# Kernel tuning notes

Hardware: AMD Instinct MI355X
Metric: run time of the kernel (lower is better)

The kernel has to match this reference:

```python
import jax, jax.numpy as jnp
import numpy as np

B, S, H, F, E, N, K = 2, 4096, 1024, 3584, 8, 2, 2


def setup_inputs() -> dict:
    key = jax.random.key(0)
    ks = jax.random.split(key, 6)
    scale_h = 1.0 / np.sqrt(H)
    scale_f = 1.0 / np.sqrt(F)
    return {
        "hidden_states": jax.random.normal(ks[0], (B, S, H), dtype=jnp.float32),
        "gate_w": jax.random.normal(ks[1], (E, H), dtype=jnp.float32) * scale_h,
        "gate2_w": jax.random.normal(ks[2], (N, H), dtype=jnp.float32) * scale_h,
        "w1": jax.random.normal(ks[3], (E, F, H), dtype=jnp.float32) * scale_h,
        "w2": jax.random.normal(ks[4], (E, H, F), dtype=jnp.float32) * scale_f,
        "w3": jax.random.normal(ks[5], (E, F, H), dtype=jnp.float32) * scale_h,
    }


def reference(hidden_states, gate_w, gate2_w, w1, w2, w3):
    b, s, h = hidden_states.shape
    x = hidden_states.reshape(-1, h)  # [T, H]

    # Router: real gate + null-expert gate, concatenated
    router_logits = jnp.concatenate([x @ gate_w.T, x @ gate2_w.T], axis=1)  # [T, E+N]
    rw = jax.nn.softmax(router_logits.astype(jnp.float32), axis=1)
    top_w, sel = jax.lax.top_k(rw, K)  # [T, K]

    # Null experts (idx >= E) get their raw weight; real experts are renormalized
    mask = sel < E
    sw = top_w * mask
    denom = sw.sum(axis=-1, keepdims=True)
    denom = jnp.where(denom == 0, 1.0, denom)
    weights = (sw / denom + top_w * (~mask)).astype(x.dtype)  # [T, K]

    # Per-(token, real-expert) combine weight; null experts drop out (one_hot -> 0)
    combine = jnp.einsum("tke,tk->et", jax.nn.one_hot(sel, E, dtype=x.dtype), weights)  # [E, T]

    def body(acc, p):
        w1e, w2e, w3e, cw = p
        hgate = jax.nn.silu(x @ w1e.T) * (x @ w3e.T)  # [T, F]
        return acc + cw[:, None] * (hgate @ w2e.T), None

    out, _ = jax.lax.scan(body, jnp.zeros_like(x), (w1, w2, w3, combine))
    return out.reshape(b, s, h), router_logits
```

## Files before the change

kernel.cpp:

```cpp
#include <hip/hip_runtime.h>
#include <hip/hip_bf16.h>

namespace {

constexpr int T_TOK = 8192;
constexpr int HDIM  = 1024;
constexpr int FDIM  = 3584;
constexpr int CAP_ROWS = 17408;
constexpr int MAXMT = CAP_ROWS / 128;

typedef __bf16 bf16x8 __attribute__((ext_vector_type(8)));
typedef float  f32x4  __attribute__((ext_vector_type(4)));
typedef float  f32x16 __attribute__((ext_vector_type(16)));

#define CFENCE() asm volatile("" ::: "memory")

__device__ inline unsigned short f2bf(float f) {
  union { float f; unsigned u; } a; a.f = f;
  unsigned r = a.u + 0x7fffu + ((a.u >> 16) & 1u);
  return (unsigned short)(r >> 16);
}

typedef const __attribute__((address_space(1))) void* gptr_t;
typedef __attribute__((address_space(3))) void* lptr_t;
__device__ inline void gload_lds16(const void* g, void* l) {
  __builtin_amdgcn_global_load_lds((gptr_t)g, (lptr_t)l, 16, 0, 0);
}

#define MFMA32(a, b, c) __builtin_amdgcn_mfma_f32_32x32x16_bf16(a, b, c, 0, 0, 0)

__global__ __launch_bounds__(256) void k_router(
    const float* __restrict__ x, const float* __restrict__ gw,
    const float* __restrict__ gw2, float* __restrict__ logits_out,
    int* __restrict__ sel, float* __restrict__ wts)
{
  int t = blockIdx.x * 4 + (threadIdx.x >> 6);
  int lane = threadIdx.x & 63;
  if (t >= T_TOK) return;
  const float* xr = x + (size_t)t * HDIM;
  float acc[10];
#pragma unroll
  for (int e = 0; e < 10; ++e) acc[e] = 0.f;
#pragma unroll
  for (int it = 0; it < 4; ++it) {
    int base = it * 256 + lane * 4;
    float4 xv = *reinterpret_cast<const float4*>(xr + base);
#pragma unroll
    for (int e = 0; e < 8; ++e) {
      float4 g = *reinterpret_cast<const float4*>(gw + e * HDIM + base);
      acc[e] += xv.x * g.x + xv.y * g.y + xv.z * g.z + xv.w * g.w;
    }
#pragma unroll
    for (int e = 0; e < 2; ++e) {
      float4 g = *reinterpret_cast<const float4*>(gw2 + e * HDIM + base);
      acc[8 + e] += xv.x * g.x + xv.y * g.y + xv.z * g.z + xv.w * g.w;
    }
  }
#pragma unroll
  for (int e = 0; e < 10; ++e) {
#pragma unroll
    for (int off = 32; off > 0; off >>= 1)
      acc[e] += __shfl_xor(acc[e], off, 64);
  }
  if (lane == 0) {
    float* lo = logits_out + (size_t)t * 10;
#pragma unroll
    for (int e = 0; e < 10; ++e) lo[e] = acc[e];
    float mx = acc[0];
#pragma unroll
    for (int e = 1; e < 10; ++e) mx = fmaxf(mx, acc[e]);
    float p[10], s = 0.f;
#pragma unroll
    for (int e = 0; e < 10; ++e) { p[e] = __expf(acc[e] - mx); s += p[e]; }
    float inv = 1.f / s;
#pragma unroll
    for (int e = 0; e < 10; ++e) p[e] *= inv;
    int i0 = 0;
    for (int e = 1; e < 10; ++e) if (p[e] > p[i0]) i0 = e;
    int i1 = (i0 == 0) ? 1 : 0;
    for (int e = 0; e < 10; ++e) if (e != i0 && p[e] > p[i1]) i1 = e;
    float w0 = p[i0], w1 = p[i1];
    bool r0 = i0 < 8, r1 = i1 < 8;
    float den = (r0 ? w0 : 0.f) + (r1 ? w1 : 0.f);
    if (den == 0.f) den = 1.f;
    sel[t * 2]     = i0; wts[t * 2]     = r0 ? w0 / den : 0.f;
    sel[t * 2 + 1] = i1; wts[t * 2 + 1] = r1 ? w1 / den : 0.f;
  }
}

__global__ __launch_bounds__(256) void k_histseg(
    const int* __restrict__ sel, int* __restrict__ meta)
{
  __shared__ int part[256][8];
  __shared__ int s_tile0[9];
  int tid = threadIdx.x;
  int c[8];
#pragma unroll
  for (int e = 0; e < 8; ++e) c[e] = 0;
  for (int i = 0; i < 64; ++i) {
    int v = sel[i * 256 + tid];
#pragma unroll
    for (int e = 0; e < 8; ++e) c[e] += (v == e);
  }
#pragma unroll
  for (int e = 0; e < 8; ++e) part[tid][e] = c[e];
  __syncthreads();
  for (int s = 128; s >= 1; s >>= 1) {
    if (tid < s) {
#pragma unroll
      for (int e = 0; e < 8; ++e) part[tid][e] += part[tid + s][e];
    }
    __syncthreads();
  }
  if (tid == 0) {
    int off = 0;
    for (int e = 0; e < 8; ++e) {
      int cnt = part[0][e];
      meta[e] = cnt;
      meta[8 + e] = 0;
      meta[16 + e] = off;
      s_tile0[e] = off >> 7;
      off += (cnt + 127) & ~127;
    }
    meta[24] = off;
    meta[25] = off >> 7;
    s_tile0[8] = off >> 7;
  }
  __syncthreads();
  int nt = s_tile0[8];
  if (tid < nt) {
    int e = 0;
    while (s_tile0[e + 1] <= tid) ++e;
    meta[32 + tid] = e;
  }
}

__global__ __launch_bounds__(256) void k_zeropad(
    const int* __restrict__ meta, unsigned short* __restrict__ xg)
{
  int e = blockIdx.x >> 7, r = blockIdx.x & 127;
  int c = meta[e];
  int pad = (c + 127) & ~127;
  if (c + r >= pad) return;
  size_t row = (size_t)meta[16 + e] + c + r;
  reinterpret_cast<ushort4*>(xg + row * HDIM)[threadIdx.x] = ushort4{0, 0, 0, 0};
}

__global__ __launch_bounds__(256) void k_scatter(
    const float* __restrict__ x, const int* __restrict__ sel,
    int* __restrict__ meta, int* __restrict__ pair_row,
    unsigned short* __restrict__ xg)
{
  __shared__ int s_cnt[8];
  __shared__ int s_base[8];
  __shared__ int s_row[256];
  int tid = threadIdx.x;
  int pair0 = blockIdx.x * 256;
  if (tid < 8) s_cnt[tid] = 0;
  __syncthreads();
  int e = sel[pair0 + tid];
  int rank = -1;
  if (e < 8) rank = atomicAdd(&s_cnt[e], 1);
  __syncthreads();
  if (tid < 8) {
    int c = s_cnt[tid];
    s_base[tid] = c > 0 ? atomicAdd(&meta[8 + tid], c) : 0;
  }
  __syncthreads();
  int row = (e < 8) ? meta[16 + e] + s_base[e] + rank : -1;
  pair_row[pair0 + tid] = row;
  s_row[tid] = row;
  __syncthreads();
  int wid = tid >> 6, lane = tid & 63;
  for (int i = wid; i < 256; i += 4) {
    int r = s_row[i];
    if (r < 0) continue;
    const float* xr = x + (size_t)((pair0 + i) >> 1) * HDIM;
    unsigned short* dst = xg + (size_t)r * HDIM;
#pragma unroll
    for (int it = 0; it < 4; ++it) {
      int base = it * 256 + lane * 4;
      float4 v = *reinterpret_cast<const float4*>(xr + base);
      ushort4 o{f2bf(v.x), f2bf(v.y), f2bf(v.z), f2bf(v.w)};
      *reinterpret_cast<ushort4*>(dst + base) = o;
    }
  }
}

__global__ __launch_bounds__(256) void k_conv3(
    const float* __restrict__ s1, const float* __restrict__ s3,
    const float* __restrict__ s2,
    unsigned short* __restrict__ d1, unsigned short* __restrict__ d3,
    unsigned short* __restrict__ d2,
    long long total, long long rl13, long long ss13,
    long long rl2, long long ss2)
{
  long long i = ((long long)blockIdx.x * 256 + threadIdx.x) * 8;
  if (i >= total) return;
  const float* src; unsigned short* dst; long long rowlen, sstride;
  if (blockIdx.y == 0)      { src = s1; dst = d1; rowlen = rl13; sstride = ss13; }
  else if (blockIdx.y == 1) { src = s3; dst = d3; rowlen = rl13; sstride = ss13; }
  else                      { src = s2; dst = d2; rowlen = rl2;  sstride = ss2;  }
  const float* sp;
  if (rowlen == sstride) {
    sp = src + i;
  } else {
    long long r = i / rowlen, c = i - r * rowlen;
    sp = src + r * sstride + c;
  }
  float4 a = reinterpret_cast<const float4*>(sp)[0];
  float4 b = reinterpret_cast<const float4*>(sp)[1];
  ushort4* d = reinterpret_cast<ushort4*>(dst + i);
  d[0] = ushort4{f2bf(a.x), f2bf(a.y), f2bf(a.z), f2bf(a.w)};
  d[1] = ushort4{f2bf(b.x), f2bf(b.y), f2bf(b.z), f2bf(b.w)};
}

__global__ __launch_bounds__(256) void k_gemm1(
    const unsigned short* __restrict__ xg,
    const unsigned short* __restrict__ wc1,
    const unsigned short* __restrict__ wc3,
    unsigned short* __restrict__ hg,
    const int* __restrict__ meta, int Fc)
{
  __shared__ unsigned short As[128 * 64];
  __shared__ unsigned short B1s[64 * 64];
  __shared__ unsigned short B3s[64 * 64];

  int mt = blockIdx.y;
  if (mt >= meta[25]) return;
  int e = meta[32 + mt];
  int mrow0 = mt * 128;
  int fl0 = blockIdx.x * 64;

  int tid = threadIdx.x, wid = tid >> 6, lane = tid & 63;
  int l31 = lane & 31, lh = lane >> 5;
  int wm = wid >> 1, wn = wid & 1;

  f32x16 acc1[2], acc3[2];
#pragma unroll
  for (int m = 0; m < 2; ++m)
#pragma unroll
    for (int j = 0; j < 16; ++j) { acc1[m][j] = 0.f; acc3[m][j] = 0.f; }

  const unsigned short* w1p = wc1 + ((size_t)e * Fc + fl0) * HDIM;
  const unsigned short* w3p = wc3 + ((size_t)e * Fc + fl0) * HDIM;

  int srow = tid >> 3;
  int sc8  = tid & 7;

  for (int k0 = 0; k0 < HDIM; k0 += 64) {
#pragma unroll
    for (int i = 0; i < 4; ++i) {
      int row = i * 32 + srow;
      int c8 = sc8 ^ (row & 7);
      gload_lds16(xg + (size_t)(mrow0 + row) * HDIM + k0 + c8 * 8,
                  (char*)As + i * 4096 + wid * 1024);
    }
#pragma unroll
    for (int i = 0; i < 2; ++i) {
      int row = i * 32 + srow;
      int c8 = sc8 ^ (row & 7);
      gload_lds16(w1p + (size_t)row * HDIM + k0 + c8 * 8,
                  (char*)B1s + i * 4096 + wid * 1024);
      gload_lds16(w3p + (size_t)row * HDIM + k0 + c8 * 8,
                  (char*)B3s + i * 4096 + wid * 1024);
    }
    __syncthreads();

#pragma unroll
    for (int ks = 0; ks < 4; ++ks) {
      int rb = wn * 32 + l31;
      int kb_b = (ks * 32 + lh * 16) ^ ((rb & 7) << 4);
      bf16x8 b1 = *reinterpret_cast<const bf16x8*>((const char*)B1s + rb * 128 + kb_b);
      bf16x8 b3 = *reinterpret_cast<const bf16x8*>((const char*)B3s + rb * 128 + kb_b);
#pragma unroll
      for (int m = 0; m < 2; ++m) {
        int ra = wm * 64 + m * 32 + l31;
        int kb_a = (ks * 32 + lh * 16) ^ ((ra & 7) << 4);
        bf16x8 a = *reinterpret_cast<const bf16x8*>((const char*)As + ra * 128 + kb_a);
        acc1[m] = MFMA32(a, b1, acc1[m]);
        acc3[m] = MFMA32(a, b3, acc3[m]);
      }
    }
    __syncthreads();
  }

#pragma unroll
  for (int m = 0; m < 2; ++m) {
    int gcol = fl0 + wn * 32 + l31;
#pragma unroll
    for (int r = 0; r < 16; ++r) {
      int grow = mrow0 + wm * 64 + m * 32 + (r & 3) + 8 * (r >> 2) + 4 * lh;
      float s1 = acc1[m][r];
      float s3 = acc3[m][r];
      float h = s1 / (1.f + __expf(-s1)) * s3;
      hg[(size_t)grow * Fc + gcol] = f2bf(h);
    }
  }
}

__global__ __launch_bounds__(256) void k_gemm2(
    const unsigned short* __restrict__ hg,
    const unsigned short* __restrict__ wc2,
    float* __restrict__ yrows, const int* __restrict__ meta,
    int Fc, int first)
{
  __shared__ __attribute__((aligned(128))) char lds[65536];

  int mt = blockIdx.y;
  if (mt >= meta[25]) return;
  int e = meta[32 + mt];
  int mrow0 = mt * 128;
  int hcol0 = blockIdx.x * 128;

  int tid = threadIdx.x, wid = tid >> 6, lane = tid & 63;
  int lr = lane & 15, lg = lane >> 4;
  int wm = wid >> 1, wn = wid & 1;

  f32x4 acc[4][4];
  const f32x4 zero = {0.f, 0.f, 0.f, 0.f};
#pragma unroll
  for (int m = 0; m < 4; ++m)
#pragma unroll
    for (int n = 0; n < 4; ++n) acc[m][n] = zero;

  const unsigned short* w2p = wc2 + ((size_t)e * HDIM + hcol0) * Fc;

  int srow = tid >> 3;
  int c8 = (tid & 7) ^ (srow & 7);

  const unsigned short* pa[4];
  const unsigned short* pb[4];
#pragma unroll
  for (int i = 0; i < 4; ++i) {
    pa[i] = hg + (size_t)(mrow0 + i * 32 + srow) * Fc + c8 * 8;
    pb[i] = w2p + (size_t)(i * 32 + srow) * Fc + c8 * 8;
  }

  auto STAGE = [&](int buf) {
    char* base = lds + buf * 32768;
#pragma unroll
    for (int i = 0; i < 4; ++i) {
      gload_lds16(pa[i], base + i * 4096 + wid * 1024);
      pa[i] += 64;
      gload_lds16(pb[i], base + 16384 + i * 4096 + wid * 1024);
      pb[i] += 64;
    }
  };

  auto COMPUTE = [&](int buf) {
    const char* base = lds + buf * 32768;
#pragma unroll
    for (int kk = 0; kk < 2; ++kk) {
      bf16x8 a[4], b[4];
#pragma unroll
      for (int m = 0; m < 4; ++m) {
        int r = wm * 64 + m * 16 + lr;
        int off = r * 128 + ((kk * 64 + lg * 16) ^ ((r & 7) << 4));
        a[m] = *reinterpret_cast<const bf16x8*>(base + off);
      }
#pragma unroll
      for (int n = 0; n < 4; ++n) {
        int r = wn * 64 + n * 16 + lr;
        int off = r * 128 + ((kk * 64 + lg * 16) ^ ((r & 7) << 4));
        b[n] = *reinterpret_cast<const bf16x8*>(base + 16384 + off);
      }
#pragma unroll
      for (int m = 0; m < 4; ++m)
#pragma unroll
        for (int n = 0; n < 4; ++n)
          acc[m][n] = __builtin_amdgcn_mfma_f32_16x16x32_bf16(a[m], b[n], acc[m][n], 0, 0, 0);
    }
  };

  int NT = Fc / 64;
  int cur = 0;
  STAGE(0);
#pragma unroll 1
  for (int t = 0; t < NT - 1; ++t) {
    STAGE(cur ^ 1);
    asm volatile("s_waitcnt vmcnt(8)" ::: "memory");
    __builtin_amdgcn_s_barrier();
    CFENCE();
    COMPUTE(cur);
    CFENCE();
    __builtin_amdgcn_s_barrier();
    cur ^= 1;
  }
  asm volatile("s_waitcnt vmcnt(0)" ::: "memory");
  __builtin_amdgcn_s_barrier();
  CFENCE();
  COMPUTE(cur);

#pragma unroll
  for (int m = 0; m < 4; ++m)
#pragma unroll
    for (int n = 0; n < 4; ++n) {
      int gcol = hcol0 + wn * 64 + n * 16 + lr;
#pragma unroll
      for (int j = 0; j < 4; ++j) {
        int grow = mrow0 + wm * 64 + m * 16 + lg * 4 + j;
        float* yp = yrows + (size_t)grow * HDIM + gcol;
        float v = acc[m][n][j];
        if (first) *yp = v; else *yp += v;
      }
    }
}

__global__ __launch_bounds__(256) void k_combine(
    const float* __restrict__ yrows, const int* __restrict__ pair_row,
    const float* __restrict__ wts, float* __restrict__ out)
{
  int t = blockIdx.x * 4 + (threadIdx.x >> 6);
  int lane = threadIdx.x & 63;
  if (t >= T_TOK) return;
  int r0 = pair_row[t * 2], r1 = pair_row[t * 2 + 1];
  float w0 = (r0 >= 0) ? wts[t * 2] : 0.f;
  float w1 = (r1 >= 0) ? wts[t * 2 + 1] : 0.f;
  const float* y0 = yrows + (size_t)(r0 >= 0 ? r0 : 0) * HDIM;
  const float* y1 = yrows + (size_t)(r1 >= 0 ? r1 : 0) * HDIM;
  float* op = out + (size_t)t * HDIM;
#pragma unroll
  for (int it = 0; it < 4; ++it) {
    int base = it * 256 + lane * 4;
    float4 a = *reinterpret_cast<const float4*>(y0 + base);
    float4 b = *reinterpret_cast<const float4*>(y1 + base);
    float4 r{w0 * a.x + w1 * b.x, w0 * a.y + w1 * b.y,
             w0 * a.z + w1 * b.z, w0 * a.w + w1 * b.w};
    *reinterpret_cast<float4*>(op + base) = r;
  }
}

}

extern "C" void kernel_launch(void* const* d_in, const int* in_sizes, int n_in,
                              void* d_out, int out_size, void* d_ws, size_t ws_size,
                              hipStream_t stream)
{
  const float* x   = (const float*)d_in[0];
  const float* gw  = (const float*)d_in[1];
  const float* gw2 = (const float*)d_in[2];
  const float* w1  = (const float*)d_in[3];
  const float* w2  = (const float*)d_in[4];
  const float* w3  = (const float*)d_in[5];
  float* out = (float*)d_out;
  float* logits_out = out + (size_t)T_TOK * HDIM;

  char* p = (char*)d_ws;
  int* meta = (int*)p;            p += 1024;
  int* sel = (int*)p;             p += T_TOK * 2 * sizeof(int);
  float* wts = (float*)p;         p += T_TOK * 2 * sizeof(float);
  int* pair_row = (int*)p;        p += T_TOK * 2 * sizeof(int);
  unsigned short* xg = (unsigned short*)p;  p += (size_t)CAP_ROWS * HDIM * 2;
  float* yrows = (float*)p;                 p += (size_t)CAP_ROWS * HDIM * 4;
  size_t fixed = (size_t)(p - (char*)d_ws);

  int nf = 28;
  const int opts[6] = {1, 2, 4, 7, 14, 28};
  for (int i = 0; i < 6; ++i) {
    size_t Fc_i = FDIM / opts[i];
    size_t need = fixed + 3 * 16384 * Fc_i + (size_t)CAP_ROWS * Fc_i * 2;
    if (need <= ws_size) { nf = opts[i]; break; }
  }
  int Fc = FDIM / nf;

  unsigned short* wc1 = (unsigned short*)p;  p += (size_t)16384 * Fc;
  unsigned short* wc3 = (unsigned short*)p;  p += (size_t)16384 * Fc;
  unsigned short* wc2 = (unsigned short*)p;  p += (size_t)16384 * Fc;
  unsigned short* hg  = (unsigned short*)p;

  k_router<<<T_TOK / 4, 256, 0, stream>>>(x, gw, gw2, logits_out, sel, wts);
  k_histseg<<<1, 256, 0, stream>>>(sel, meta);
  k_zeropad<<<1024, 256, 0, stream>>>(meta, xg);
  k_scatter<<<T_TOK * 2 / 256, 256, 0, stream>>>(x, sel, meta, pair_row, xg);

  long long total = 8LL * Fc * HDIM;
  int ncb = (int)(total / 8 / 256);
  for (int c = 0; c < nf; ++c) {
    long long c0 = (long long)c * Fc;
    k_conv3<<<dim3(ncb, 3), 256, 0, stream>>>(
        w1 + c0 * HDIM, w3 + c0 * HDIM, w2 + c0, wc1, wc3, wc2,
        total, (long long)Fc * HDIM, (long long)FDIM * HDIM,
        (long long)Fc, (long long)FDIM);

    k_gemm1<<<dim3(Fc / 64, MAXMT), 256, 0, stream>>>(xg, wc1, wc3, hg, meta, Fc);
    k_gemm2<<<dim3(HDIM / 128, MAXMT), 256, 0, stream>>>(hg, wc2, yrows, meta, Fc, c == 0 ? 1 : 0);
  }
  k_combine<<<T_TOK / 4, 256, 0, stream>>>(yrows, pair_row, wts, out);
}
```

Baseline: 527.5 us.

## Widen gemm1 N-tile to 128 and switch to 16x16x32 MFMA

The gate/up GEMM tile grows from 128x64 to 128x128 per block, so each loaded A tile is reused across twice as many F columns and the grid is halved. The inner loop moves from 32x32x16 MFMAs to a 4x4 grid of 16x16x32 MFMAs per wave, with matching fragment loads and epilogue indexing. This doubles the accumulator registers (two 4x4 sets of f32x4) and the LDS for the B tiles, which may reduce occupancy. It requires Fc to be divisible by 128.

New measurement: 705.4 us. +33.7%, slower.

```diff
diff --git a/kernel.cpp b/kernel.cpp
--- a/kernel.cpp
+++ b/kernel.cpp
@@ -11,7 +11,6 @@
 
 typedef __bf16 bf16x8 __attribute__((ext_vector_type(8)));
 typedef float  f32x4  __attribute__((ext_vector_type(4)));
-typedef float  f32x16 __attribute__((ext_vector_type(16)));
 
 #define CFENCE() asm volatile("" ::: "memory")
 
@@ -27,7 +26,7 @@
   __builtin_amdgcn_global_load_lds((gptr_t)g, (lptr_t)l, 16, 0, 0);
 }
 
-#define MFMA32(a, b, c) __builtin_amdgcn_mfma_f32_32x32x16_bf16(a, b, c, 0, 0, 0)
+#define MFMA16(a, b, c) __builtin_amdgcn_mfma_f32_16x16x32_bf16(a, b, c, 0, 0, 0)
 
 __global__ __launch_bounds__(256) void k_router(
     const float* __restrict__ x, const float* __restrict__ gw,
@@ -223,24 +222,25 @@
     const int* __restrict__ meta, int Fc)
 {
   __shared__ unsigned short As[128 * 64];
-  __shared__ unsigned short B1s[64 * 64];
-  __shared__ unsigned short B3s[64 * 64];
+  __shared__ unsigned short B1s[128 * 64];
+  __shared__ unsigned short B3s[128 * 64];
 
   int mt = blockIdx.y;
   if (mt >= meta[25]) return;
   int e = meta[32 + mt];
   int mrow0 = mt * 128;
-  int fl0 = blockIdx.x * 64;
+  int fl0 = blockIdx.x * 128;
 
   int tid = threadIdx.x, wid = tid >> 6, lane = tid & 63;
-  int l31 = lane & 31, lh = lane >> 5;
+  int lr = lane & 15, lg = lane >> 4;
   int wm = wid >> 1, wn = wid & 1;
 
-  f32x16 acc1[2], acc3[2];
-#pragma unroll
-  for (int m = 0; m < 2; ++m)
-#pragma unroll
-    for (int j = 0; j < 16; ++j) { acc1[m][j] = 0.f; acc3[m][j] = 0.f; }
+  f32x4 acc1[4][4], acc3[4][4];
+  const f32x4 zero = {0.f, 0.f, 0.f, 0.f};
+#pragma unroll
+  for (int m = 0; m < 4; ++m)
+#pragma unroll
+    for (int n = 0; n < 4; ++n) { acc1[m][n] = zero; acc3[m][n] = zero; }
 
   const unsigned short* w1p = wc1 + ((size_t)e * Fc + fl0) * HDIM;
   const unsigned short* w3p = wc3 + ((size_t)e * Fc + fl0) * HDIM;
@@ -255,11 +255,6 @@
       int c8 = sc8 ^ (row & 7);
       gload_lds16(xg + (size_t)(mrow0 + row) * HDIM + k0 + c8 * 8,
                   (char*)As + i * 4096 + wid * 1024);
-    }
-#pragma unroll
-    for (int i = 0; i < 2; ++i) {
-      int row = i * 32 + srow;
-      int c8 = sc8 ^ (row & 7);
       gload_lds16(w1p + (size_t)row * HDIM + k0 + c8 * 8,
                   (char*)B1s + i * 4096 + wid * 1024);
       gload_lds16(w3p + (size_t)row * HDIM + k0 + c8 * 8,
@@ -268,35 +263,44 @@
     __syncthreads();
 
 #pragma unroll
-    for (int ks = 0; ks < 4; ++ks) {
-      int rb = wn * 32 + l31;
-      int kb_b = (ks * 32 + lh * 16) ^ ((rb & 7) << 4);
-      bf16x8 b1 = *reinterpret_cast<const bf16x8*>((const char*)B1s + rb * 128 + kb_b);
-      bf16x8 b3 = *reinterpret_cast<const bf16x8*>((const char*)B3s + rb * 128 + kb_b);
-#pragma unroll
-      for (int m = 0; m < 2; ++m) {
-        int ra = wm * 64 + m * 32 + l31;
-        int kb_a = (ks * 32 + lh * 16) ^ ((ra & 7) << 4);
-        bf16x8 a = *reinterpret_cast<const bf16x8*>((const char*)As + ra * 128 + kb_a);
-        acc1[m] = MFMA32(a, b1, acc1[m]);
-        acc3[m] = MFMA32(a, b3, acc3[m]);
+    for (int kk = 0; kk < 2; ++kk) {
+      bf16x8 a[4];
+#pragma unroll
+      for (int m = 0; m < 4; ++m) {
+        int r = wm * 64 + m * 16 + lr;
+        int off = r * 128 + ((kk * 64 + lg * 16) ^ ((r & 7) << 4));
+        a[m] = *reinterpret_cast<const bf16x8*>((const char*)As + off);
+      }
+#pragma unroll
+      for (int n = 0; n < 4; ++n) {
+        int r = wn * 64 + n * 16 + lr;
+        int off = r * 128 + ((kk * 64 + lg * 16) ^ ((r & 7) << 4));
+        bf16x8 b1 = *reinterpret_cast<const bf16x8*>((const char*)B1s + off);
+        bf16x8 b3 = *reinterpret_cast<const bf16x8*>((const char*)B3s + off);
+#pragma unroll
+        for (int m = 0; m < 4; ++m) {
+          acc1[m][n] = MFMA16(a[m], b1, acc1[m][n]);
+          acc3[m][n] = MFMA16(a[m], b3, acc3[m][n]);
+        }
       }
     }
     __syncthreads();
   }
 
 #pragma unroll
-  for (int m = 0; m < 2; ++m) {
-    int gcol = fl0 + wn * 32 + l31;
-#pragma unroll
-    for (int r = 0; r < 16; ++r) {
-      int grow = mrow0 + wm * 64 + m * 32 + (r & 3) + 8 * (r >> 2) + 4 * lh;
-      float s1 = acc1[m][r];
-      float s3 = acc3[m][r];
-      float h = s1 / (1.f + __expf(-s1)) * s3;
-      hg[(size_t)grow * Fc + gcol] = f2bf(h);
-    }
-  }
+  for (int m = 0; m < 4; ++m)
+#pragma unroll
+    for (int n = 0; n < 4; ++n) {
+      int gcol = fl0 + wn * 64 + n * 16 + lr;
+#pragma unroll
+      for (int j = 0; j < 4; ++j) {
+        int grow = mrow0 + wm * 64 + m * 16 + lg * 4 + j;
+        float s1 = acc1[m][n][j];
+        float s3 = acc3[m][n][j];
+        float h = s1 / (1.f + __expf(-s1)) * s3;
+        hg[(size_t)grow * Fc + gcol] = f2bf(h);
+      }
+    }
 }
 
 __global__ __launch_bounds__(256) void k_gemm2(
@@ -369,7 +373,7 @@
       for (int m = 0; m < 4; ++m)
 #pragma unroll
         for (int n = 0; n < 4; ++n)
-          acc[m][n] = __builtin_amdgcn_mfma_f32_16x16x32_bf16(a[m], b[n], acc[m][n], 0, 0, 0);
+          acc[m][n] = MFMA16(a[m], b[n], acc[m][n]);
     }
   };
 
@@ -483,7 +487,7 @@
         total, (long long)Fc * HDIM, (long long)FDIM * HDIM,
         (long long)Fc, (long long)FDIM);
 
-    k_gemm1<<<dim3(Fc / 64, MAXMT), 256, 0, stream>>>(xg, wc1, wc3, hg, meta, Fc);
+    k_gemm1<<<dim3(Fc / 128, MAXMT), 256, 0, stream>>>(xg, wc1, wc3, hg, meta, Fc);
     k_gemm2<<<dim3(HDIM / 128, MAXMT), 256, 0, stream>>>(hg, wc2, yrows, meta, Fc, c == 0 ? 1 : 0);
   }
   k_combine<<<T_TOK / 4, 256, 0, stream>>>(yrows, pair_row, wts, out);
```
